# Optimization experiments

Measured on AMD Instinct MI355X. Metric: run time of the kernel, lower is better.

The kernel has to match this reference:

```python
import jax, jax.numpy as jnp
import numpy as np

EMBED_DIM = 1024
NUM_HEADS = 16
HEAD_DIM = EMBED_DIM // NUM_HEADS


def setup_inputs() -> dict:
    key = jax.random.key(0)
    ks = jax.random.split(key, 7)
    B, N, C = 2, 2048, EMBED_DIM
    s = 1.0 / np.sqrt(C)
    return {
        "x": jax.random.normal(ks[0], (B, N, C), dtype=jnp.float32),
        "phase_signal": jax.random.uniform(ks[1], (B,), dtype=jnp.float32),
        "qkv_w": jax.random.normal(ks[2], (3 * C, C), dtype=jnp.float32) * s,
        "qkv_b": jnp.zeros((3 * C,), dtype=jnp.float32),
        "proj_w": jax.random.normal(ks[3], (C, C), dtype=jnp.float32) * s,
        "proj_b": jnp.zeros((C,), dtype=jnp.float32),
        "phase_weight": jnp.ones((NUM_HEADS,), dtype=jnp.float32),
    }


def reference(x, phase_signal, qkv_w, qkv_b, proj_w, proj_b, phase_weight):
    B, N, C = x.shape
    H, D = NUM_HEADS, HEAD_DIM
    # qkv projection: [B,N,3C] -> [3,B,H,N,D]
    qkv = (x @ qkv_w.T + qkv_b).reshape(B, N, 3, H, D)
    qkv = jnp.transpose(qkv, (2, 0, 3, 1, 4))
    q, k, v = qkv[0], qkv[1], qkv[2]
    attn = jnp.einsum("bhnd,bhmd->bhnm", q, k) * (D ** -0.5)
    # per-(batch, head) phase modulation applied before softmax
    phase_mod = phase_weight[None, :, None, None] * phase_signal[:, None, None, None]
    attn = attn * (1.0 + 0.2 * phase_mod)
    attn = jax.nn.softmax(attn, axis=-1)  # dropout is identity in eval mode
    out = jnp.einsum("bhnm,bhmd->bhnd", attn, v)
    out = jnp.transpose(out, (0, 2, 1, 3)).reshape(B, N, C)
    return out @ proj_w.T + proj_b
```

## Files before the change

### kernel.cpp

```cpp
#include <hip/hip_runtime.h>
#include <stdint.h>

#define NUM_H 16
#define HD    64
#define CDIM  1024
#define NSEQ  2048
#define NBATCH 2
#define LOG2E 1.4426950408889634f

typedef __attribute__((ext_vector_type(8))) short short8;
typedef __attribute__((ext_vector_type(4))) float f32x4;
typedef __attribute__((ext_vector_type(16))) float f32x16;
typedef __attribute__((ext_vector_type(4))) unsigned short ushort4v;
typedef __attribute__((ext_vector_type(4))) float float4v;
typedef __attribute__((ext_vector_type(2))) unsigned int u32x2;

__device__ __forceinline__ unsigned short f2bf(float f) {
    unsigned int u = __builtin_bit_cast(unsigned int, f);
    unsigned int r = u + 0x7fffu + ((u >> 16) & 1u);
    return (unsigned short)(r >> 16);
}

__device__ __forceinline__ unsigned int cvtpk(float a, float b) {
    unsigned int r;
    asm("v_cvt_pk_bf16_f32 %0, %1, %2" : "=v"(r) : "v"(a), "v"(b));
    return r;
}

__device__ __forceinline__ void plswap(unsigned int &a, unsigned int &b) {
    asm("v_permlane32_swap_b32 %0, %1" : "+v"(a), "+v"(b));
}

__device__ __forceinline__ void gload_lds16(const void* g, const void* l) {
    __builtin_amdgcn_global_load_lds(
        (const __attribute__((address_space(1))) unsigned int*)(unsigned long long)(uintptr_t)g,
        (__attribute__((address_space(3))) unsigned int*)(unsigned int)(uintptr_t)l,
        16, 0, 0);
}

__global__ void cvt_bf16_kernel(const float* __restrict__ in,
                                unsigned short* __restrict__ out, int n4) {
    int i = blockIdx.x * blockDim.x + threadIdx.x;
    if (i < n4) {
        float4v v = *(const float4v*)(in + (size_t)i * 4);
        ushort4v o;
        o[0] = f2bf(v[0]); o[1] = f2bf(v[1]); o[2] = f2bf(v[2]); o[3] = f2bf(v[3]);
        *(ushort4v*)(out + (size_t)i * 4) = o;
    }
}

__global__ __launch_bounds__(512, 2) void gemm_qkv(
    const unsigned short* __restrict__ A,
    const unsigned short* __restrict__ Bw,
    const float* __restrict__ bias,
    const float* __restrict__ ps,
    const float* __restrict__ pw,
    unsigned short* __restrict__ qb,
    unsigned short* __restrict__ kb,
    unsigned short* __restrict__ vtb)
{
    __shared__ unsigned short lds[2][2][2][128][64];

    const int tid = threadIdx.x;
    const int wid = tid >> 6;
    const int lane = tid & 63;
    const int l15 = lane & 15, l4 = lane >> 4;
    const int wave_m = wid >> 2, wave_n = wid & 3;

    const int bm = blockIdx.x;
    const int bn = blockIdx.y;

    f32x4 acc[8][4];
    const f32x4 zero4 = {0.f, 0.f, 0.f, 0.f};
#pragma unroll
    for (int m = 0; m < 8; ++m)
#pragma unroll
        for (int n = 0; n < 4; ++n) acc[m][n] = zero4;

    const int jr = lane >> 3;
    const int jc = ((lane & 7) ^ jr) << 4;
    const char* aB = (const char*)A  + (size_t)(bm * 256) * 2048;
    const char* bB = (const char*)Bw + (size_t)(bn * 256) * 2048;

    auto stageH = [&](int t, int which) {
        const int buf = t & 1;
        const int op = which >> 1, hf = which & 1;
        const char* src = (op == 0) ? aB : bB;
        const int rowb = hf * 128 + wid * 16;
        const size_t k0b = (size_t)t * 128;
        char* dst = (char*)&lds[buf][op][hf][wid * 16][0];
#pragma unroll
        for (int i = 0; i < 2; ++i)
            gload_lds16(src + (size_t)(rowb + i * 8 + jr) * 2048 + k0b + jc,
                        dst + i * 1024);
    };

    const int swz = (l15 & 7) << 4;
    auto rdA = [&](int buf, int mq, int mp, int kk) -> short8 {
        return *(const short8*)((const char*)&lds[buf][0][wave_m][mq * 64 + mp * 16 + l15][0]
                                + ((kk * 64 + l4 * 16) ^ swz));
    };
    auto rdB = [&](int buf, int nq, int np, int kk) -> short8 {
        const int br = wave_n * 64 + nq * 32 + np * 16 + l15;
        return *(const short8*)((const char*)&lds[buf][1][br >> 7][br & 127][0]
                                + ((kk * 64 + l4 * 16) ^ swz));
    };

    stageH(0, 0); stageH(0, 1); stageH(0, 2); stageH(0, 3);
    stageH(1, 2); stageH(1, 3); stageH(1, 0); stageH(1, 1);
    asm volatile("s_waitcnt vmcnt(8)" ::: "memory");
    __builtin_amdgcn_s_barrier();

    for (int t = 0; t < 16; ++t) {
        const int buf = t & 1;
        short8 af[4][2], bf[2][2][2];

#pragma unroll
        for (int mp = 0; mp < 4; ++mp) {
            af[mp][0] = rdA(buf, 0, mp, 0); af[mp][1] = rdA(buf, 0, mp, 1);
        }
#pragma unroll
        for (int np = 0; np < 2; ++np) {
            bf[0][np][0] = rdB(buf, 0, np, 0); bf[0][np][1] = rdB(buf, 0, np, 1);
        }
        __builtin_amdgcn_s_barrier();
        __builtin_amdgcn_s_setprio(1);
#pragma unroll
        for (int mp = 0; mp < 4; ++mp)
#pragma unroll
            for (int np = 0; np < 2; ++np)
#pragma unroll
                for (int kk = 0; kk < 2; ++kk)
                    acc[mp][np] = __builtin_amdgcn_mfma_f32_16x16x32_bf16(
                        af[mp][kk], bf[0][np][kk], acc[mp][np], 0, 0, 0);
        __builtin_amdgcn_s_setprio(0);
        __builtin_amdgcn_s_barrier();

#pragma unroll
        for (int np = 0; np < 2; ++np) {
            bf[1][np][0] = rdB(buf, 1, np, 0); bf[1][np][1] = rdB(buf, 1, np, 1);
        }
        if (t < 14) stageH(t + 2, 2);
        __builtin_amdgcn_s_barrier();
        __builtin_amdgcn_s_setprio(1);
#pragma unroll
        for (int mp = 0; mp < 4; ++mp)
#pragma unroll
            for (int np = 0; np < 2; ++np)
#pragma unroll
                for (int kk = 0; kk < 2; ++kk)
                    acc[mp][2 + np] = __builtin_amdgcn_mfma_f32_16x16x32_bf16(
                        af[mp][kk], bf[1][np][kk], acc[mp][2 + np], 0, 0, 0);
        __builtin_amdgcn_s_setprio(0);
        __builtin_amdgcn_s_barrier();

#pragma unroll
        for (int mp = 0; mp < 4; ++mp) {
            af[mp][0] = rdA(buf, 1, mp, 0); af[mp][1] = rdA(buf, 1, mp, 1);
        }
        if (t < 14) stageH(t + 2, 3);
        __builtin_amdgcn_s_barrier();
        __builtin_amdgcn_s_setprio(1);
#pragma unroll
        for (int mp = 0; mp < 4; ++mp)
#pragma unroll
            for (int np = 0; np < 2; ++np)
#pragma unroll
                for (int kk = 0; kk < 2; ++kk)
                    acc[4 + mp][np] = __builtin_amdgcn_mfma_f32_16x16x32_bf16(
                        af[mp][kk], bf[0][np][kk], acc[4 + mp][np], 0, 0, 0);
        __builtin_amdgcn_s_setprio(0);
        __builtin_amdgcn_s_barrier();

        if (t < 14) { stageH(t + 2, 0); stageH(t + 2, 1); }
        __builtin_amdgcn_s_barrier();
        __builtin_amdgcn_s_setprio(1);
#pragma unroll
        for (int mp = 0; mp < 4; ++mp)
#pragma unroll
            for (int np = 0; np < 2; ++np)
#pragma unroll
                for (int kk = 0; kk < 2; ++kk)
                    acc[4 + mp][2 + np] = __builtin_amdgcn_mfma_f32_16x16x32_bf16(
                        af[mp][kk], bf[1][np][kk], acc[4 + mp][2 + np], 0, 0, 0);
        __builtin_amdgcn_s_setprio(0);
        if (t < 14)       { asm volatile("s_waitcnt vmcnt(8)" ::: "memory"); }
        else if (t == 14) { asm volatile("s_waitcnt vmcnt(0)" ::: "memory"); }
        __builtin_amdgcn_s_barrier();
    }

    const int row_base = bm * 256 + wave_m * 128;
    const int col_base = bn * 256 + wave_n * 64;
    const int t3b = bn >> 2;
    const float ps0 = ps[0], ps1 = ps[1];

    if (t3b < 2) {
        unsigned short* dstb = (t3b == 0) ? qb : kb;
#pragma unroll
        for (int n = 0; n < 4; ++n) {
            const int col3 = col_base + n * 16 + l15;
            const float bv = bias[col3];
            const int hh = (col3 >> 6) & 15;
            const int dd = col3 & 63;
            float kf0 = 1.f, kf1 = 1.f;
            if (t3b == 1) {
                const float base = 0.125f * LOG2E;
                const float pwh = pw[hh];
                kf0 = base * (1.f + 0.2f * pwh * ps0);
                kf1 = base * (1.f + 0.2f * pwh * ps1);
            }
#pragma unroll
            for (int m = 0; m < 8; ++m) {
#pragma unroll
                for (int r = 0; r < 4; ++r) {
                    const int row = row_base + m * 16 + l4 * 4 + r;
                    const int bb = row >> 11, nn = row & 2047;
                    const size_t bh = (size_t)(bb * 16 + hh);
                    float v = acc[m][n][r] + bv;
                    if (t3b == 1) v *= (bb == 0) ? kf0 : kf1;
                    dstb[(bh * 2048 + nn) * 64 + dd] = f2bf(v);
                }
            }
        }
    } else {
        unsigned short* tb = &lds[0][0][0][0][0];
        __syncthreads();
#pragma unroll
        for (int n = 0; n < 4; ++n) {
            const int col = wave_n * 64 + n * 16 + l15;
            const float bv = bias[col_base + n * 16 + l15];
            const int swzc = (col & 15) << 4;
#pragma unroll
            for (int m = 0; m < 8; ++m) {
#pragma unroll
                for (int r = 0; r < 4; ++r) {
                    const int row = wave_m * 128 + m * 16 + l4 * 4 + r;
                    *(unsigned short*)((char*)tb + col * 512 + ((row * 2) ^ swzc)) =
                        f2bf(acc[m][n][r] + bv);
                }
            }
        }
        __syncthreads();
        const int bb = bm >> 3;
        const size_t ncol0 = (size_t)(bm & 7) * 256;
#pragma unroll
        for (int i = 0; i < 16; ++i) {
            const int col = i * 16 + (tid >> 5);
            const int chunk = tid & 31;
            const short8 v = *(const short8*)((const char*)tb + col * 512 +
                                              ((chunk * 16) ^ ((col & 15) << 4)));
            const int hh = (bn & 3) * 4 + (col >> 6);
            const int dd = col & 63;
            *(short8*)(vtb + ((size_t)(bb * 16 + hh) * 64 + dd) * 2048 + ncol0 + chunk * 8) = v;
        }
    }
}

__global__ __launch_bounds__(256, 2) void gemm_proj(
    const unsigned short* __restrict__ A,
    const unsigned short* __restrict__ Bw,
    const float* __restrict__ bias,
    float* __restrict__ out)
{
    __shared__ unsigned short As[2][128 * 64];
    __shared__ unsigned short Bs[2][128 * 64];
    const int tid = threadIdx.x;
    const int wid = tid >> 6;
    const int lane = tid & 63;
    const int l15 = lane & 15, l4 = lane >> 4;
    const int bm = blockIdx.x, bn = blockIdx.y;
    const int wr = wid >> 1, wc = wid & 1;

    f32x4 acc[4][4];
    const f32x4 zero4 = {0.f, 0.f, 0.f, 0.f};
#pragma unroll
    for (int m = 0; m < 4; ++m)
#pragma unroll
        for (int n = 0; n < 4; ++n) acc[m][n] = zero4;

    const int jr = lane >> 3;
    const int jc = ((lane & 7) ^ jr) << 4;
    const char* aB = (const char*)A  + (size_t)(bm * 128) * 2048;
    const char* bB = (const char*)Bw + (size_t)(bn * 128) * 2048;

    auto stage = [&](int buf, int k0) {
#pragma unroll
        for (int i = 0; i < 4; ++i) {
            const int rowb = wid * 32 + i * 8;
            gload_lds16(aB + (size_t)(rowb + jr) * 2048 + k0 * 2 + jc,
                        (const char*)&As[buf][0] + rowb * 128);
            gload_lds16(bB + (size_t)(rowb + jr) * 2048 + k0 * 2 + jc,
                        (const char*)&Bs[buf][0] + rowb * 128);
        }
    };

    const int swz = (l15 & 7) << 4;

    stage(0, 0);
    for (int it = 0; it < 16; ++it) {
        const int buf = it & 1;
        __syncthreads();
        if (it < 15) stage(buf ^ 1, (it + 1) * 64);
#pragma unroll
        for (int kk = 0; kk < 2; ++kk) {
            short8 a[4], b[4];
#pragma unroll
            for (int m = 0; m < 4; ++m)
                a[m] = *(const short8*)((const char*)&As[buf][0] +
                        (wr * 64 + m * 16 + l15) * 128 + ((kk * 64 + l4 * 16) ^ swz));
#pragma unroll
            for (int n = 0; n < 4; ++n)
                b[n] = *(const short8*)((const char*)&Bs[buf][0] +
                        (wc * 64 + n * 16 + l15) * 128 + ((kk * 64 + l4 * 16) ^ swz));
            __builtin_amdgcn_s_setprio(1);
#pragma unroll
            for (int m = 0; m < 4; ++m)
#pragma unroll
                for (int n = 0; n < 4; ++n)
                    acc[m][n] = __builtin_amdgcn_mfma_f32_16x16x32_bf16(a[m], b[n], acc[m][n], 0, 0, 0);
            __builtin_amdgcn_s_setprio(0);
        }
    }

    const int row_base = bm * 128 + wr * 64;
    const int col_base = bn * 128 + wc * 64;
#pragma unroll
    for (int n = 0; n < 4; ++n) {
        const int col = col_base + n * 16 + l15;
        const float bv = bias[col];
#pragma unroll
        for (int m = 0; m < 4; ++m) {
#pragma unroll
            for (int r = 0; r < 4; ++r) {
                const int row = row_base + m * 16 + l4 * 4 + r;
                out[(size_t)row * 1024 + col] = acc[m][n][r] + bv;
            }
        }
    }
}

__global__ __launch_bounds__(256, 2) void attn_kernel(
    const unsigned short* __restrict__ qb,
    const unsigned short* __restrict__ kb,
    const unsigned short* __restrict__ vtb,
    unsigned short* __restrict__ aout)
{
    __shared__ unsigned short KVs[2][2][64 * 64];

    const int tid = threadIdx.x;
    const int w = tid >> 6;
    const int l = tid & 63;
    const int l31 = l & 31;
    const int hi = l >> 5;

    const int bid = blockIdx.y * 16 + blockIdx.x;
    const int wg = (bid & 7) * 64 + (bid >> 3);
    const int bh = wg >> 4;
    const int b = bh >> 4, h = bh & 15;
    const int q0 = (wg & 15) * 128 + w * 32;

    const char* qg = (const char*)(qb + (size_t)bh * 2048 * 64);
    const char* kg = (const char*)(kb + (size_t)bh * 2048 * 64);
    const char* vg = (const char*)(vtb + (size_t)bh * 64 * 2048);

    short8 qf[4];
#pragma unroll
    for (int t = 0; t < 4; ++t)
        qf[t] = *(const short8*)(qg + (size_t)(q0 + l31) * 128 + t * 32 + hi * 16);

    f32x16 oacc[2];
#pragma unroll
    for (int dt = 0; dt < 2; ++dt)
#pragma unroll
        for (int r = 0; r < 16; ++r) oacc[dt][r] = 0.f;
    float lr = 0.f;

    const int jr = l >> 3;
    const int jc = ((l & 7) ^ jr) << 4;
    auto stage = [&](int buf, int kv0) {
#pragma unroll
        for (int i = 0; i < 2; ++i) {
            const int row = w * 16 + i * 8;
            gload_lds16(kg + (size_t)(kv0 + row + jr) * 128 + jc,
                        (const char*)&KVs[buf][0][0] + row * 128);
            gload_lds16(vg + (size_t)(row + jr) * 4096 + (size_t)kv0 * 2 + jc,
                        (const char*)&KVs[buf][1][0] + row * 128);
        }
    };

    stage(0, 0);
    __syncthreads();

    const int swz = (l31 & 7) << 4;

    for (int it = 0; it < 32; ++it) {
        const int buf = it & 1;
        if (it < 31) stage(buf ^ 1, (it + 1) * 64);

        const char* Kb = (const char*)&KVs[buf][0][0];
        const char* Vb = (const char*)&KVs[buf][1][0];

        f32x16 sa[2];
        __builtin_amdgcn_s_setprio(1);
#pragma unroll
        for (int s = 0; s < 2; ++s) {
#pragma unroll
            for (int r = 0; r < 16; ++r) sa[s][r] = 0.f;
#pragma unroll
            for (int t = 0; t < 4; ++t) {
                const short8 kf = *(const short8*)(Kb + (s * 32 + l31) * 128 +
                                                   ((t * 32 + hi * 16) ^ swz));
                sa[s] = __builtin_amdgcn_mfma_f32_32x32x16_bf16(kf, qf[t], sa[s], 0, 0, 0);
            }
        }
        __builtin_amdgcn_s_setprio(0);

#pragma unroll
        for (int s = 0; s < 2; ++s)
#pragma unroll
            for (int r = 0; r < 16; ++r)
                sa[s][r] = __builtin_amdgcn_exp2f(sa[s][r] - 20.0f);

        float ts[16];
#pragma unroll
        for (int r = 0; r < 16; ++r) ts[r] = sa[0][r] + sa[1][r];
#pragma unroll
        for (int d = 8; d >= 1; d >>= 1)
#pragma unroll
            for (int r = 0; r < 8; ++r)
                if (r < d) ts[r] += ts[r + d];
        lr += ts[0] + __shfl_xor(ts[0], 32);

#pragma unroll
        for (int s = 0; s < 2; ++s) {
            unsigned int wv[8];
#pragma unroll
            for (int g = 0; g < 8; ++g)
                wv[g] = cvtpk(sa[s][g * 2], sa[s][g * 2 + 1]);
            plswap(wv[0], wv[2]); plswap(wv[1], wv[3]);
            plswap(wv[4], wv[6]); plswap(wv[5], wv[7]);
            union { unsigned int u[4]; short8 s8; } f0, f1;
            f0.u[0] = wv[0]; f0.u[1] = wv[1]; f0.u[2] = wv[2]; f0.u[3] = wv[3];
            f1.u[0] = wv[4]; f1.u[1] = wv[5]; f1.u[2] = wv[6]; f1.u[3] = wv[7];
            __builtin_amdgcn_s_setprio(1);
#pragma unroll
            for (int dt = 0; dt < 2; ++dt) {
                const short8 v0 = *(const short8*)(Vb + (dt * 32 + l31) * 128 +
                                                   (((s * 2 + 0) * 32 + hi * 16) ^ swz));
                oacc[dt] = __builtin_amdgcn_mfma_f32_32x32x16_bf16(v0, f0.s8, oacc[dt], 0, 0, 0);
                const short8 v1 = *(const short8*)(Vb + (dt * 32 + l31) * 128 +
                                                   (((s * 2 + 1) * 32 + hi * 16) ^ swz));
                oacc[dt] = __builtin_amdgcn_mfma_f32_32x32x16_bf16(v1, f1.s8, oacc[dt], 0, 0, 0);
            }
            __builtin_amdgcn_s_setprio(0);
        }
        __syncthreads();
    }

    const float inv = 1.0f / lr;
    char* outp = (char*)aout + ((size_t)(b * 2048 + q0 + l31) * 1024 + h * 64) * 2;
#pragma unroll
    for (int dt = 0; dt < 2; ++dt)
#pragma unroll
        for (int rg = 0; rg < 4; ++rg) {
            u32x2 pkd;
            pkd[0] = cvtpk(oacc[dt][rg * 4 + 0] * inv, oacc[dt][rg * 4 + 1] * inv);
            pkd[1] = cvtpk(oacc[dt][rg * 4 + 2] * inv, oacc[dt][rg * 4 + 3] * inv);
            *(u32x2*)(outp + (size_t)(dt * 32 + rg * 8 + hi * 4) * 2) = pkd;
        }
}

extern "C" void kernel_launch(void* const* d_in, const int* in_sizes, int n_in,
                              void* d_out, int out_size, void* d_ws, size_t ws_size,
                              hipStream_t stream) {
    const float* x      = (const float*)d_in[0];
    const float* ps     = (const float*)d_in[1];
    const float* qkv_w  = (const float*)d_in[2];
    const float* qkv_b  = (const float*)d_in[3];
    const float* proj_w = (const float*)d_in[4];
    const float* proj_b = (const float*)d_in[5];
    const float* pw     = (const float*)d_in[6];
    float* out = (float*)d_out;
    char* ws = (char*)d_ws;

    unsigned short* x_bf    = (unsigned short*)(ws);
    unsigned short* w1_bf   = (unsigned short*)(ws + (8u  << 20));
    unsigned short* wp_bf   = (unsigned short*)(ws + (14u << 20));
    unsigned short* qb      = (unsigned short*)(ws + (16u << 20));
    unsigned short* kb      = (unsigned short*)(ws + (24u << 20));
    unsigned short* vtb     = (unsigned short*)(ws + (32u << 20));
    unsigned short* attn_bf = x_bf;

    cvt_bf16_kernel<<<4096, 256, 0, stream>>>(x,      x_bf,  1048576);
    cvt_bf16_kernel<<<3072, 256, 0, stream>>>(qkv_w,  w1_bf, 786432);
    cvt_bf16_kernel<<<1024, 256, 0, stream>>>(proj_w, wp_bf, 262144);

    gemm_qkv<<<dim3(16, 12), 512, 0, stream>>>(x_bf, w1_bf, qkv_b, ps, pw, qb, kb, vtb);
    attn_kernel<<<dim3(16, 32), 256, 0, stream>>>(qb, kb, vtb, attn_bf);
    gemm_proj<<<dim3(32, 8), 256, 0, stream>>>(attn_bf, wp_bf, proj_b, out);
}
```

Measured before the change: 111.9 us.

## Store K and V in MFMA fragment order so attention loads are contiguous

The QKV GEMM epilogue now stages results through LDS and writes K and V to global memory pre-arranged in the exact per-lane MFMA fragment layout. Q is also staged through LDS, so its stores become coalesced 16-byte writes. In the attention kernel, K/V tile loads become fully contiguous 16-byte-per-lane copies, and LDS fragment reads use a simple lane-linear address with no swizzle arithmetic. The aim is to cut address computation and bank conflicts in the attention inner loop and to make the epilogue writes coalesced. In exchange, the epilogue adds an extra LDS round trip and barrier.

```diff
diff --git a/kernel.cpp b/kernel.cpp
--- a/kernel.cpp
+++ b/kernel.cpp
@@ -56,8 +56,8 @@
     const float* __restrict__ ps,
     const float* __restrict__ pw,
     unsigned short* __restrict__ qb,
-    unsigned short* __restrict__ kb,
-    unsigned short* __restrict__ vtb)
+    unsigned short* __restrict__ kfrag,
+    unsigned short* __restrict__ vfrag)
 {
     __shared__ unsigned short lds[2][2][2][128][64];
 
@@ -189,69 +189,95 @@
         __builtin_amdgcn_s_barrier();
     }
 
-    const int row_base = bm * 256 + wave_m * 128;
     const int col_base = bn * 256 + wave_n * 64;
     const int t3b = bn >> 2;
-    const float ps0 = ps[0], ps1 = ps[1];
-
-    if (t3b < 2) {
-        unsigned short* dstb = (t3b == 0) ? qb : kb;
+    const int bb = bm >> 3;
+    const int nn0 = (bm & 7) * 256;
+    char* tbc = (char*)&lds[0][0][0][0][0];
+
+    __syncthreads();
+
+    if (t3b == 0) {
 #pragma unroll
         for (int n = 0; n < 4; ++n) {
-            const int col3 = col_base + n * 16 + l15;
-            const float bv = bias[col3];
-            const int hh = (col3 >> 6) & 15;
-            const int dd = col3 & 63;
-            float kf0 = 1.f, kf1 = 1.f;
-            if (t3b == 1) {
-                const float base = 0.125f * LOG2E;
-                const float pwh = pw[hh];
-                kf0 = base * (1.f + 0.2f * pwh * ps0);
-                kf1 = base * (1.f + 0.2f * pwh * ps1);
-            }
+            const int d = n * 16 + l15;
+            const float bv = bias[col_base + n * 16 + l15];
 #pragma unroll
             for (int m = 0; m < 8; ++m) {
 #pragma unroll
                 for (int r = 0; r < 4; ++r) {
-                    const int row = row_base + m * 16 + l4 * 4 + r;
-                    const int bb = row >> 11, nn = row & 2047;
-                    const size_t bh = (size_t)(bb * 16 + hh);
-                    float v = acc[m][n][r] + bv;
-                    if (t3b == 1) v *= (bb == 0) ? kf0 : kf1;
-                    dstb[(bh * 2048 + nn) * 64 + dd] = f2bf(v);
+                    const int tt = wave_m * 128 + m * 16 + l4 * 4 + r;
+                    *(unsigned short*)(tbc + wave_n * 32768 + tt * 128 +
+                                       ((d * 2) ^ ((tt & 7) << 4))) = f2bf(acc[m][n][r] + bv);
                 }
             }
         }
+        __syncthreads();
+#pragma unroll
+        for (int i = 0; i < 16; ++i) {
+            const int hq = i >> 2, sub = i & 3;
+            const int tt = sub * 64 + (tid >> 3);
+            const int chunk = tid & 7;
+            const short8 v = *(const short8*)(tbc + hq * 32768 + tt * 128 +
+                                              ((chunk * 16) ^ ((tt & 7) << 4)));
+            *(short8*)(qb + ((size_t)(bb * 16 + bn * 4 + hq) * 2048 + nn0 + tt) * 64 + chunk * 8) = v;
+        }
+    } else if (t3b == 1) {
+        const float ps0 = ps[0], ps1 = ps[1];
+        const int hh = (bn - 4) * 4 + wave_n;
+        const float kf = 0.125f * LOG2E *
+                         (1.f + 0.2f * pw[hh] * ((bb == 0) ? ps0 : ps1));
+#pragma unroll
+        for (int n = 0; n < 4; ++n) {
+            const int hi_ = l15 >> 3, e = l15 & 7;
+            const float bv = bias[col_base + n * 16 + l15];
+#pragma unroll
+            for (int m = 0; m < 8; ++m) {
+#pragma unroll
+                for (int r = 0; r < 4; ++r) {
+                    const int tt = wave_m * 128 + m * 16 + l4 * 4 + r;
+                    const int ti = tt >> 6, u = tt & 63;
+                    const int s_ = u >> 5, l31_ = u & 31;
+                    *(unsigned short*)(tbc + (((wave_n * 4 + ti) * 8 + s_ * 4 + n) << 10) +
+                                       ((hi_ * 32 + l31_) << 4) + e * 2) =
+                        f2bf((acc[m][n][r] + bv) * kf);
+                }
+            }
+        }
+        __syncthreads();
+#pragma unroll
+        for (int i = 0; i < 16; ++i) {
+            const int hq = i >> 2, ti = i & 3;
+            const short8 v = *(const short8*)(tbc + i * 8192 + tid * 16);
+            *(short8*)(kfrag + ((size_t)(bb * 16 + (bn - 4) * 4 + hq) * 32 +
+                                ((bm & 7) * 4 + ti)) * 4096 + tid * 8) = v;
+        }
     } else {
-        unsigned short* tb = &lds[0][0][0][0][0];
-        __syncthreads();
 #pragma unroll
         for (int n = 0; n < 4; ++n) {
-            const int col = wave_n * 64 + n * 16 + l15;
+            const int d = n * 16 + l15;
+            const int dt_ = n >> 1, l31_ = d & 31;
             const float bv = bias[col_base + n * 16 + l15];
-            const int swzc = (col & 15) << 4;
 #pragma unroll
             for (int m = 0; m < 8; ++m) {
 #pragma unroll
                 for (int r = 0; r < 4; ++r) {
-                    const int row = wave_m * 128 + m * 16 + l4 * 4 + r;
-                    *(unsigned short*)((char*)tb + col * 512 + ((row * 2) ^ swzc)) =
+                    const int tt = wave_m * 128 + m * 16 + l4 * 4 + r;
+                    const int ti = tt >> 6, u = tt & 63;
+                    const int ks = u >> 4, hi_ = (u >> 3) & 1, e = u & 7;
+                    *(unsigned short*)(tbc + (((wave_n * 4 + ti) * 8 + dt_ * 4 + ks) << 10) +
+                                       ((hi_ * 32 + l31_) << 4) + e * 2) =
                         f2bf(acc[m][n][r] + bv);
                 }
             }
         }
         __syncthreads();
-        const int bb = bm >> 3;
-        const size_t ncol0 = (size_t)(bm & 7) * 256;
 #pragma unroll
         for (int i = 0; i < 16; ++i) {
-            const int col = i * 16 + (tid >> 5);
-            const int chunk = tid & 31;
-            const short8 v = *(const short8*)((const char*)tb + col * 512 +
-                                              ((chunk * 16) ^ ((col & 15) << 4)));
-            const int hh = (bn & 3) * 4 + (col >> 6);
-            const int dd = col & 63;
-            *(short8*)(vtb + ((size_t)(bb * 16 + hh) * 64 + dd) * 2048 + ncol0 + chunk * 8) = v;
+            const int hq = i >> 2, ti = i & 3;
+            const short8 v = *(const short8*)(tbc + i * 8192 + tid * 16);
+            *(short8*)(vfrag + ((size_t)(bb * 16 + (bn - 8) * 4 + hq) * 32 +
+                                ((bm & 7) * 4 + ti)) * 4096 + tid * 8) = v;
         }
     }
 }
@@ -341,11 +367,11 @@
 
 __global__ __launch_bounds__(256, 2) void attn_kernel(
     const unsigned short* __restrict__ qb,
-    const unsigned short* __restrict__ kb,
-    const unsigned short* __restrict__ vtb,
+    const unsigned short* __restrict__ kfrag,
+    const unsigned short* __restrict__ vfrag,
     unsigned short* __restrict__ aout)
 {
-    __shared__ unsigned short KVs[2][2][64 * 64];
+    __shared__ unsigned short KVs[2][2][4096];
 
     const int tid = threadIdx.x;
     const int w = tid >> 6;
@@ -360,8 +386,8 @@
     const int q0 = (wg & 15) * 128 + w * 32;
 
     const char* qg = (const char*)(qb + (size_t)bh * 2048 * 64);
-    const char* kg = (const char*)(kb + (size_t)bh * 2048 * 64);
-    const char* vg = (const char*)(vtb + (size_t)bh * 64 * 2048);
+    const unsigned short* kg = kfrag + (size_t)bh * 32 * 4096;
+    const unsigned short* vg = vfrag + (size_t)bh * 32 * 4096;
 
     short8 qf[4];
 #pragma unroll
@@ -375,30 +401,24 @@
         for (int r = 0; r < 16; ++r) oacc[dt][r] = 0.f;
     float lr = 0.f;
 
-    const int jr = l >> 3;
-    const int jc = ((l & 7) ^ jr) << 4;
-    auto stage = [&](int buf, int kv0) {
+    auto stage = [&](int buf, int T) {
 #pragma unroll
         for (int i = 0; i < 2; ++i) {
-            const int row = w * 16 + i * 8;
-            gload_lds16(kg + (size_t)(kv0 + row + jr) * 128 + jc,
-                        (const char*)&KVs[buf][0][0] + row * 128);
-            gload_lds16(vg + (size_t)(row + jr) * 4096 + (size_t)kv0 * 2 + jc,
-                        (const char*)&KVs[buf][1][0] + row * 128);
+            const int c = w * 2 + i;
+            gload_lds16(kg + (size_t)T * 4096 + c * 512 + l * 8, &KVs[buf][0][c * 512]);
+            gload_lds16(vg + (size_t)T * 4096 + c * 512 + l * 8, &KVs[buf][1][c * 512]);
         }
     };
 
     stage(0, 0);
     __syncthreads();
 
-    const int swz = (l31 & 7) << 4;
-
     for (int it = 0; it < 32; ++it) {
         const int buf = it & 1;
-        if (it < 31) stage(buf ^ 1, (it + 1) * 64);
-
-        const char* Kb = (const char*)&KVs[buf][0][0];
-        const char* Vb = (const char*)&KVs[buf][1][0];
+        if (it < 31) stage(buf ^ 1, it + 1);
+
+        const unsigned short* Kb = &KVs[buf][0][0];
+        const unsigned short* Vb = &KVs[buf][1][0];
 
         f32x16 sa[2];
         __builtin_amdgcn_s_setprio(1);
@@ -408,8 +428,7 @@
             for (int r = 0; r < 16; ++r) sa[s][r] = 0.f;
 #pragma unroll
             for (int t = 0; t < 4; ++t) {
-                const short8 kf = *(const short8*)(Kb + (s * 32 + l31) * 128 +
-                                                   ((t * 32 + hi * 16) ^ swz));
+                const short8 kf = *(const short8*)(Kb + (s * 4 + t) * 512 + l * 8);
                 sa[s] = __builtin_amdgcn_mfma_f32_32x32x16_bf16(kf, qf[t], sa[s], 0, 0, 0);
             }
         }
@@ -445,11 +464,9 @@
             __builtin_amdgcn_s_setprio(1);
 #pragma unroll
             for (int dt = 0; dt < 2; ++dt) {
-                const short8 v0 = *(const short8*)(Vb + (dt * 32 + l31) * 128 +
-                                                   (((s * 2 + 0) * 32 + hi * 16) ^ swz));
+                const short8 v0 = *(const short8*)(Vb + (dt * 4 + s * 2 + 0) * 512 + l * 8);
                 oacc[dt] = __builtin_amdgcn_mfma_f32_32x32x16_bf16(v0, f0.s8, oacc[dt], 0, 0, 0);
-                const short8 v1 = *(const short8*)(Vb + (dt * 32 + l31) * 128 +
-                                                   (((s * 2 + 1) * 32 + hi * 16) ^ swz));
+                const short8 v1 = *(const short8*)(Vb + (dt * 4 + s * 2 + 1) * 512 + l * 8);
                 oacc[dt] = __builtin_amdgcn_mfma_f32_32x32x16_bf16(v1, f1.s8, oacc[dt], 0, 0, 0);
             }
             __builtin_amdgcn_s_setprio(0);
@@ -487,15 +504,15 @@
     unsigned short* w1_bf   = (unsigned short*)(ws + (8u  << 20));
     unsigned short* wp_bf   = (unsigned short*)(ws + (14u << 20));
     unsigned short* qb      = (unsigned short*)(ws + (16u << 20));
-    unsigned short* kb      = (unsigned short*)(ws + (24u << 20));
-    unsigned short* vtb     = (unsigned short*)(ws + (32u << 20));
+    unsigned short* kfrag   = (unsigned short*)(ws + (24u << 20));
+    unsigned short* vfrag   = (unsigned short*)(ws + (32u << 20));
     unsigned short* attn_bf = x_bf;
 
     cvt_bf16_kernel<<<4096, 256, 0, stream>>>(x,      x_bf,  1048576);
     cvt_bf16_kernel<<<3072, 256, 0, stream>>>(qkv_w,  w1_bf, 786432);
     cvt_bf16_kernel<<<1024, 256, 0, stream>>>(proj_w, wp_bf, 262144);
 
-    gemm_qkv<<<dim3(16, 12), 512, 0, stream>>>(x_bf, w1_bf, qkv_b, ps, pw, qb, kb, vtb);
-    attn_kernel<<<dim3(16, 32), 256, 0, stream>>>(qb, kb, vtb, attn_bf);
+    gemm_qkv<<<dim3(16, 12), 512, 0, stream>>>(x_bf, w1_bf, qkv_b, ps, pw, qb, kfrag, vfrag);
+    attn_kernel<<<dim3(16, 32), 256, 0, stream>>>(qb, kfrag, vfrag, attn_bf);
     gemm_proj<<<dim3(32, 8), 256, 0, stream>>>(attn_bf, wp_bf, proj_b, out);
 }
```

Result: no change. 110.1 us (-1.6%).
